# Performance work log

Hardware: AMD Instinct MI355X
Metric: run time of the kernel (lower is better)

The kernel has to match this reference:

```python
import jax, jax.numpy as jnp
import numpy as np

NUM_ITEMS = 100000
OUT_DIM = 128
BATCH = 16384
HIST = 50
TOTAL = BATCH * HIST


def setup_inputs() -> dict:
    key = jax.random.key(0)
    k1, k2, k3, k4, k5, k6 = jax.random.split(key, 6)
    feature_ids = jax.random.randint(k1, (TOTAL,), 0, NUM_ITEMS + 1, dtype=jnp.int64 if jax.config.jax_enable_x64 else jnp.int32)
    # ratings in {0.5, 1.0, ..., 5.0} so that (r - 0.5) * 2 is an int index in [0, 10)
    ratings = jax.random.randint(k2, (TOTAL,), 0, 10).astype(jnp.float32) / 2.0 + 0.5
    segment_ids = jnp.repeat(jnp.arange(BATCH, dtype=jnp.int32), HIST)  # [TOTAL]
    item_ids = jax.random.randint(k3, (BATCH,), 0, NUM_ITEMS, dtype=jnp.int32)
    # kaiming_uniform_(a=sqrt(5)) on an [N, D] table -> U(-b, b) with b = sqrt(6 / ((1 + 5) * D)) = 1/sqrt(D)
    b = 1.0 / np.sqrt(OUT_DIM)
    user_W = jax.random.uniform(k4, (NUM_ITEMS + 1, OUT_DIM), jnp.float32, -b, b)
    rating_W = jax.random.uniform(k5, (10, OUT_DIM), jnp.float32, -b, b)
    item_W = jax.random.uniform(k6, (NUM_ITEMS, OUT_DIM), jnp.float32, -b, b)
    bias = jnp.zeros((OUT_DIM,), jnp.float32)
    return {"feature_ids": feature_ids, "ratings": ratings, "segment_ids": segment_ids,
            "item_ids": item_ids, "user_W": user_W, "rating_W": rating_W,
            "item_W": item_W, "bias": bias}


def reference(feature_ids, ratings, segment_ids, item_ids, user_W, rating_W, item_W, bias):
    batch = item_ids.shape[0]
    rating_idx = ((ratings - 0.5) * 2.0).astype(jnp.int32)          # [T], in [0, 10)
    rating_weights = rating_W[rating_idx]                            # [T, D] gather
    user_weights = user_W[feature_ids] * rating_weights              # [T, D] gather + multiply
    user_sum = jax.ops.segment_sum(user_weights, segment_ids, num_segments=batch)  # [B, D]
    return user_sum + item_W[item_ids] + bias                        # [B, D]
```

## Files before the change

### kernel.cpp

```cpp
#include <hip/hip_runtime.h>


#define BATCH     16384
#define HIST      50
#define UNROLL    10
#define DIM4      32
#define ROWS      8
#define BLOCK     256
#define NROWS_U   100001
#define N4_TBL    (NROWS_U * DIM4)

struct __attribute__((aligned(8))) half4 { _Float16 x, y, z, w; };

__global__ __launch_bounds__(256) void convert_kernel(
    const float4* __restrict__ src, half4* __restrict__ dst, int n4)
{
    int i = blockIdx.x * blockDim.x + threadIdx.x;
    const int stride = gridDim.x * blockDim.x;
    for (; i < n4; i += stride) {
        const float4 v = src[i];
        half4 h;
        h.x = (_Float16)v.x; h.y = (_Float16)v.y;
        h.z = (_Float16)v.z; h.w = (_Float16)v.w;
        dst[i] = h;
    }
}

__global__ __launch_bounds__(BLOCK) void features_linear_h16(
    const int*    __restrict__ feature_ids,
    const float*  __restrict__ ratings,
    const int*    __restrict__ item_ids,
    const half4*  __restrict__ user_h,
    const float4* __restrict__ rating_W,
    const float4* __restrict__ item_W,
    const float4* __restrict__ bias,
    float4*       __restrict__ out)
{
    __shared__ float4 sh_rW[10 * DIM4];
    __shared__ int    sh_fid[ROWS * HIST];
    __shared__ int    sh_ridx[ROWS * HIST];

    const int tid = threadIdx.x;

    for (int i = tid; i < 10 * DIM4; i += BLOCK) sh_rW[i] = rating_W[i];

    const int base = blockIdx.x * (ROWS * HIST);
    for (int i = tid; i < ROWS * HIST; i += BLOCK) {
        sh_fid[i] = feature_ids[base + i];
        float r = ratings[base + i];
        sh_ridx[i] = (int)(r * 2.0f) - 1;
    }
    __syncthreads();

    const int row = tid >> 5;
    const int d4  = tid & 31;
    const int b   = blockIdx.x * ROWS + row;

    float4 acc; acc.x = 0.f; acc.y = 0.f; acc.z = 0.f; acc.w = 0.f;
    const int off = row * HIST;

    for (int h = 0; h < HIST; h += UNROLL) {
        int f[UNROLL], r[UNROLL];
#pragma unroll
        for (int i = 0; i < UNROLL; ++i) {
            f[i] = sh_fid[off + h + i];
            r[i] = sh_ridx[off + h + i];
        }

        half4 u[UNROLL];
#pragma unroll
        for (int i = 0; i < UNROLL; ++i) {
            u[i] = user_h[f[i] * DIM4 + d4];
        }

#pragma unroll
        for (int i = 0; i < UNROLL; ++i) {
            const float4 w = sh_rW[r[i] * DIM4 + d4];
            acc.x += (float)u[i].x * w.x;
            acc.y += (float)u[i].y * w.y;
            acc.z += (float)u[i].z * w.z;
            acc.w += (float)u[i].w * w.w;
        }
    }

    const int    iid = item_ids[b];
    const float4 iw  = item_W[iid * DIM4 + d4];
    const float4 bs  = bias[d4];

    float4 o;
    o.x = acc.x + iw.x + bs.x;
    o.y = acc.y + iw.y + bs.y;
    o.z = acc.z + iw.z + bs.z;
    o.w = acc.w + iw.w + bs.w;
    out[b * DIM4 + d4] = o;
}

__global__ __launch_bounds__(BLOCK) void features_linear_f32(
    const int*    __restrict__ feature_ids,
    const float*  __restrict__ ratings,
    const int*    __restrict__ item_ids,
    const float4* __restrict__ user_W,
    const float4* __restrict__ rating_W,
    const float4* __restrict__ item_W,
    const float4* __restrict__ bias,
    float4*       __restrict__ out)
{
    __shared__ float4 sh_rW[10 * DIM4];
    __shared__ int    sh_fid[ROWS * HIST];
    __shared__ int    sh_ridx[ROWS * HIST];

    const int tid = threadIdx.x;
    for (int i = tid; i < 10 * DIM4; i += BLOCK) sh_rW[i] = rating_W[i];
    const int base = blockIdx.x * (ROWS * HIST);
    for (int i = tid; i < ROWS * HIST; i += BLOCK) {
        sh_fid[i] = feature_ids[base + i];
        float r = ratings[base + i];
        sh_ridx[i] = (int)(r * 2.0f) - 1;
    }
    __syncthreads();

    const int row = tid >> 5;
    const int d4  = tid & 31;
    const int b   = blockIdx.x * ROWS + row;

    float4 acc; acc.x = 0.f; acc.y = 0.f; acc.z = 0.f; acc.w = 0.f;
    const int off = row * HIST;

    for (int h = 0; h < HIST; h += UNROLL) {
        int f[UNROLL], r[UNROLL];
#pragma unroll
        for (int i = 0; i < UNROLL; ++i) {
            f[i] = sh_fid[off + h + i];
            r[i] = sh_ridx[off + h + i];
        }
        float4 u[UNROLL];
#pragma unroll
        for (int i = 0; i < UNROLL; ++i) u[i] = user_W[f[i] * DIM4 + d4];
#pragma unroll
        for (int i = 0; i < UNROLL; ++i) {
            const float4 w = sh_rW[r[i] * DIM4 + d4];
            acc.x += u[i].x * w.x;
            acc.y += u[i].y * w.y;
            acc.z += u[i].z * w.z;
            acc.w += u[i].w * w.w;
        }
    }

    const int    iid = item_ids[b];
    const float4 iw  = item_W[iid * DIM4 + d4];
    const float4 bs  = bias[d4];

    float4 o;
    o.x = acc.x + iw.x + bs.x;
    o.y = acc.y + iw.y + bs.y;
    o.z = acc.z + iw.z + bs.z;
    o.w = acc.w + iw.w + bs.w;
    out[b * DIM4 + d4] = o;
}

extern "C" void kernel_launch(void* const* d_in, const int* in_sizes, int n_in,
                              void* d_out, int out_size, void* d_ws, size_t ws_size,
                              hipStream_t stream) {
    const int*    feature_ids = (const int*)   d_in[0];
    const float*  ratings     = (const float*) d_in[1];
    const int*    item_ids    = (const int*)   d_in[3];
    const float4* user_W      = (const float4*)d_in[4];
    const float4* rating_W    = (const float4*)d_in[5];
    const float4* item_W      = (const float4*)d_in[6];
    const float4* bias        = (const float4*)d_in[7];
    float4*       out         = (float4*)      d_out;

    dim3 grid(BATCH / ROWS);
    dim3 block(BLOCK);

    const size_t need = (size_t)N4_TBL * sizeof(half4);
    if (d_ws != nullptr && ws_size >= need) {
        half4* user_h = (half4*)d_ws;
        convert_kernel<<<dim3(4096), dim3(256), 0, stream>>>(
            user_W, user_h, N4_TBL);
        features_linear_h16<<<grid, block, 0, stream>>>(
            feature_ids, ratings, item_ids, user_h, rating_W, item_W, bias, out);
    } else {
        features_linear_f32<<<grid, block, 0, stream>>>(
            feature_ids, ratings, item_ids, user_W, rating_W, item_W, bias, out);
    }
}
```

Measured before the change: 164.1 us.

## Slice fp16 user table by dimension and pack ids with rating index

The conversion kernel now writes the fp16 user table as 8 column slices of 16 dims each, so every slice is a compact 3.2 MB table. It also packs feature id and rating index into one int per history entry. The main kernel assigns one slice per block (slice = blockIdx & 7) with 64 batch rows per block, so consecutive blocks gather from the same small slice. This is meant to keep the gather working set cache-resident. In exchange each gather reads only 32 bytes per row, and the packed ids are read eight times.

```diff
diff --git a/kernel.cpp b/kernel.cpp
--- a/kernel.cpp
+++ b/kernel.cpp
@@ -3,79 +3,94 @@
 
 #define BATCH     16384
 #define HIST      50
+#define TOTAL     (BATCH * HIST)
 #define UNROLL    10
 #define DIM4      32
-#define ROWS      8
+#define NROWS_U   100001
+#define SLICES    8
+#define SL_H4     (NROWS_U * 4)
+#define UT_H4     (SLICES * SL_H4)
+#define UT_BYTES  ((size_t)UT_H4 * 8)
+#define RPB       64
 #define BLOCK     256
-#define NROWS_U   100001
-#define N4_TBL    (NROWS_U * DIM4)
 
 struct __attribute__((aligned(8))) half4 { _Float16 x, y, z, w; };
 
-__global__ __launch_bounds__(256) void convert_kernel(
-    const float4* __restrict__ src, half4* __restrict__ dst, int n4)
-{
-    int i = blockIdx.x * blockDim.x + threadIdx.x;
-    const int stride = gridDim.x * blockDim.x;
-    for (; i < n4; i += stride) {
-        const float4 v = src[i];
-        half4 h;
-        h.x = (_Float16)v.x; h.y = (_Float16)v.y;
-        h.z = (_Float16)v.z; h.w = (_Float16)v.w;
-        dst[i] = h;
-    }
-}
-
-__global__ __launch_bounds__(BLOCK) void features_linear_h16(
+__global__ __launch_bounds__(256) void convert_pack_kernel(
+    const float4* __restrict__ src,
     const int*    __restrict__ feature_ids,
     const float*  __restrict__ ratings,
+    half4*        __restrict__ uT,
+    int*          __restrict__ packed)
+{
+    const int tid = blockIdx.x * 256 + threadIdx.x;
+    const int stride = gridDim.x * 256;
+    if (blockIdx.y < SLICES) {
+        const int slice = blockIdx.y;
+        half4* dst = uT + (size_t)slice * SL_H4;
+        for (int i = tid; i < SL_H4; i += stride) {
+            const int row = i >> 2, d = i & 3;
+            const float4 v = src[row * DIM4 + slice * 4 + d];
+            half4 h;
+            h.x = (_Float16)v.x; h.y = (_Float16)v.y;
+            h.z = (_Float16)v.z; h.w = (_Float16)v.w;
+            dst[i] = h;
+        }
+    } else {
+        for (int t = tid; t < TOTAL; t += stride) {
+            const int fid  = feature_ids[t];
+            const int ridx = (int)(ratings[t] * 2.0f) - 1;
+            packed[t] = (fid << 4) | ridx;
+        }
+    }
+}
+
+__global__ __launch_bounds__(BLOCK) void features_linear_sliced(
+    const int*    __restrict__ packed,
     const int*    __restrict__ item_ids,
-    const half4*  __restrict__ user_h,
+    const half4*  __restrict__ uT,
     const float4* __restrict__ rating_W,
     const float4* __restrict__ item_W,
     const float4* __restrict__ bias,
     float4*       __restrict__ out)
 {
-    __shared__ float4 sh_rW[10 * DIM4];
-    __shared__ int    sh_fid[ROWS * HIST];
-    __shared__ int    sh_ridx[ROWS * HIST];
-
-    const int tid = threadIdx.x;
-
-    for (int i = tid; i < 10 * DIM4; i += BLOCK) sh_rW[i] = rating_W[i];
-
-    const int base = blockIdx.x * (ROWS * HIST);
-    for (int i = tid; i < ROWS * HIST; i += BLOCK) {
-        sh_fid[i] = feature_ids[base + i];
-        float r = ratings[base + i];
-        sh_ridx[i] = (int)(r * 2.0f) - 1;
-    }
+    __shared__ int    sh_pid[RPB * HIST];
+    __shared__ float4 sh_rW[10 * 4];
+
+    const int tid   = threadIdx.x;
+    const int slice = blockIdx.x & 7;
+    const int grp   = blockIdx.x >> 3;
+
+    if (tid < 40)
+        sh_rW[tid] = rating_W[(tid >> 2) * DIM4 + slice * 4 + (tid & 3)];
+
+    const int base = grp * (RPB * HIST);
+    for (int i = tid; i < RPB * HIST; i += BLOCK)
+        sh_pid[i] = packed[base + i];
     __syncthreads();
 
-    const int row = tid >> 5;
-    const int d4  = tid & 31;
-    const int b   = blockIdx.x * ROWS + row;
+    const int row = tid >> 2;
+    const int d   = tid & 3;
+    const int b   = grp * RPB + row;
+    const int off = row * HIST;
+
+    const half4* us = uT + (size_t)slice * SL_H4;
 
     float4 acc; acc.x = 0.f; acc.y = 0.f; acc.z = 0.f; acc.w = 0.f;
-    const int off = row * HIST;
 
     for (int h = 0; h < HIST; h += UNROLL) {
-        int f[UNROLL], r[UNROLL];
+        int p[UNROLL];
+#pragma unroll
+        for (int i = 0; i < UNROLL; ++i) p[i] = sh_pid[off + h + i];
+
+        half4 u[UNROLL];
+#pragma unroll
+        for (int i = 0; i < UNROLL; ++i)
+            u[i] = us[(p[i] >> 4) * 4 + d];
+
 #pragma unroll
         for (int i = 0; i < UNROLL; ++i) {
-            f[i] = sh_fid[off + h + i];
-            r[i] = sh_ridx[off + h + i];
-        }
-
-        half4 u[UNROLL];
-#pragma unroll
-        for (int i = 0; i < UNROLL; ++i) {
-            u[i] = user_h[f[i] * DIM4 + d4];
-        }
-
-#pragma unroll
-        for (int i = 0; i < UNROLL; ++i) {
-            const float4 w = sh_rW[r[i] * DIM4 + d4];
+            const float4 w = sh_rW[(p[i] & 15) * 4 + d];
             acc.x += (float)u[i].x * w.x;
             acc.y += (float)u[i].y * w.y;
             acc.z += (float)u[i].z * w.z;
@@ -84,15 +99,15 @@
     }
 
     const int    iid = item_ids[b];
-    const float4 iw  = item_W[iid * DIM4 + d4];
-    const float4 bs  = bias[d4];
+    const float4 iw  = item_W[iid * DIM4 + slice * 4 + d];
+    const float4 bs  = bias[slice * 4 + d];
 
     float4 o;
     o.x = acc.x + iw.x + bs.x;
     o.y = acc.y + iw.y + bs.y;
     o.z = acc.z + iw.z + bs.z;
     o.w = acc.w + iw.w + bs.w;
-    out[b * DIM4 + d4] = o;
+    out[b * DIM4 + slice * 4 + d] = o;
 }
 
 __global__ __launch_bounds__(BLOCK) void features_linear_f32(
@@ -106,13 +121,13 @@
     float4*       __restrict__ out)
 {
     __shared__ float4 sh_rW[10 * DIM4];
-    __shared__ int    sh_fid[ROWS * HIST];
-    __shared__ int    sh_ridx[ROWS * HIST];
+    __shared__ int    sh_fid[8 * HIST];
+    __shared__ int    sh_ridx[8 * HIST];
 
     const int tid = threadIdx.x;
     for (int i = tid; i < 10 * DIM4; i += BLOCK) sh_rW[i] = rating_W[i];
-    const int base = blockIdx.x * (ROWS * HIST);
-    for (int i = tid; i < ROWS * HIST; i += BLOCK) {
+    const int base = blockIdx.x * (8 * HIST);
+    for (int i = tid; i < 8 * HIST; i += BLOCK) {
         sh_fid[i] = feature_ids[base + i];
         float r = ratings[base + i];
         sh_ridx[i] = (int)(r * 2.0f) - 1;
@@ -121,7 +136,7 @@
 
     const int row = tid >> 5;
     const int d4  = tid & 31;
-    const int b   = blockIdx.x * ROWS + row;
+    const int b   = blockIdx.x * 8 + row;
 
     float4 acc; acc.x = 0.f; acc.y = 0.f; acc.z = 0.f; acc.w = 0.f;
     const int off = row * HIST;
@@ -170,18 +185,18 @@
     const float4* bias        = (const float4*)d_in[7];
     float4*       out         = (float4*)      d_out;
 
-    dim3 grid(BATCH / ROWS);
-    dim3 block(BLOCK);
-
-    const size_t need = (size_t)N4_TBL * sizeof(half4);
+    const size_t need = UT_BYTES + (size_t)TOTAL * sizeof(int);
     if (d_ws != nullptr && ws_size >= need) {
-        half4* user_h = (half4*)d_ws;
-        convert_kernel<<<dim3(4096), dim3(256), 0, stream>>>(
-            user_W, user_h, N4_TBL);
-        features_linear_h16<<<grid, block, 0, stream>>>(
-            feature_ids, ratings, item_ids, user_h, rating_W, item_W, bias, out);
+        half4* uT     = (half4*)d_ws;
+        int*   packed = (int*)((char*)d_ws + UT_BYTES);
+
+        convert_pack_kernel<<<dim3(784, 9), dim3(256), 0, stream>>>(
+            user_W, feature_ids, ratings, uT, packed);
+
+        features_linear_sliced<<<dim3((BATCH / RPB) * SLICES), dim3(BLOCK), 0, stream>>>(
+            packed, item_ids, uT, rating_W, item_W, bias, out);
     } else {
-        features_linear_f32<<<grid, block, 0, stream>>>(
+        features_linear_f32<<<dim3(BATCH / 8), dim3(BLOCK), 0, stream>>>(
             feature_ids, ratings, item_ids, user_W, rating_W, item_W, bias, out);
     }
 }
```

New measurement: 174.6 us. +6.4%, slower.
